# Kernel optimization log

Hardware: AMD Instinct MI355X
Metric: run time of the kernel (lower is better)

The kernel has to match this reference:

```python
import jax, jax.numpy as jnp
import numpy as np

K = 12          # number of agents (== max_other_agents, required by blowup)
MOA = 12        # max_other_agents
H, W, D = 24, 24, 8
C0, C1, C2, C3 = 32, 16, 16, 8
PHYS, MENT, ACT = 16, 16, 16
HSZ = C3 * H * W                      # 4608
INP = HSZ + PHYS + MENT + MOA * PHYS + MOA * MENT  # 5024
EPS = 1e-5
MIX = 0.9


def setup_inputs() -> dict:
    key = jax.random.key(0)
    ks = jax.random.split(key, 32)
    s = 0.02
    d = {
        "x": jax.random.normal(ks[0], (K, C0, D, H, W), jnp.float32),
        "p": jax.random.normal(ks[1], (K, PHYS), jnp.float32),
        "m": jax.random.normal(ks[2], (K, MENT), jnp.float32),
        "vis": jax.random.uniform(ks[3], (K, MOA), jnp.float32),
        "conv1_w": jax.random.normal(ks[4], (C1, C0, D), jnp.float32) * s,
        "conv1_b": jnp.zeros((C1,), jnp.float32),
        "bn1_g": jnp.ones((C1,), jnp.float32),
        "bn1_b": jnp.zeros((C1,), jnp.float32),
        "conv2_w": jax.random.normal(ks[5], (C2, C1, 3, 3), jnp.float32) * s,
        "conv2_b": jnp.zeros((C2,), jnp.float32),
        "bn2_g": jnp.ones((C2,), jnp.float32),
        "bn2_b": jnp.zeros((C2,), jnp.float32),
        "conv3_w": jax.random.normal(ks[6], (C3, C2, 5, 5), jnp.float32) * s,
        "conv3_b": jnp.zeros((C3,), jnp.float32),
        "bn3_g": jnp.ones((C3,), jnp.float32),
        "bn3_b": jnp.zeros((C3,), jnp.float32),
        "phys_w": jax.random.normal(ks[7], (PHYS, PHYS), jnp.float32) * s,
        "phys_b": jnp.zeros((PHYS,), jnp.float32),
        "ment_w": jax.random.normal(ks[8], (MENT, MENT), jnp.float32) * s,
        "ment_b": jnp.zeros((MENT,), jnp.float32),
        "w_ih": jax.random.normal(ks[9], (4 * HSZ, INP), jnp.float32) * s,
        "w_hh": jax.random.normal(ks[10], (4 * HSZ, HSZ), jnp.float32) * s,
        "b_ih": jnp.zeros((4 * HSZ,), jnp.float32),
        "b_hh": jnp.zeros((4 * HSZ,), jnp.float32),
        "ah_w": jax.random.normal(ks[11], (128, HSZ), jnp.float32) * s,
        "ah_b": jnp.zeros((128,), jnp.float32),
        "act_w": jax.random.normal(ks[12], (ACT, 128), jnp.float32) * s,
        "act_b": jnp.zeros((ACT,), jnp.float32),
        "inf_w": jax.random.normal(ks[13], (MOA * MENT, HSZ), jnp.float32) * s,
        "inf_b": jnp.zeros((MOA * MENT,), jnp.float32),
    }
    return d


def _bn2d(x, g, b):
    # batch-norm in training mode (batch statistics, biased var), x: [N,C,H,W]
    mu = jnp.mean(x, axis=(0, 2, 3), keepdims=True)
    var = jnp.mean((x - mu) ** 2, axis=(0, 2, 3), keepdims=True)
    return (x - mu) * jax.lax.rsqrt(var + EPS) * g[None, :, None, None] + b[None, :, None, None]


def _conv2d(x, w, b):
    y = jax.lax.conv_general_dilated(x, w, (1, 1), 'SAME',
                                     dimension_numbers=('NCHW', 'OIHW', 'NCHW'))
    return y + b[None, :, None, None]


def reference(x, p, m, vis,
              conv1_w, conv1_b, bn1_g, bn1_b,
              conv2_w, conv2_b, bn2_g, bn2_b,
              conv3_w, conv3_b, bn3_g, bn3_b,
              phys_w, phys_b, ment_w, ment_b,
              w_ih, w_hh, b_ih, b_hh,
              ah_w, ah_b, act_w, act_b, inf_w, inf_b):
    k = K
    # Conv3d with kernel (D,1,1) == contraction over channel and depth dims
    h1 = jnp.einsum('bcdhw,ocd->bohw', x, conv1_w) + conv1_b[None, :, None, None]
    h1 = jax.nn.relu(_bn2d(h1, bn1_g, bn1_b))          # [k,C1,H,W]
    h2 = jax.nn.relu(_bn2d(_conv2d(h1, conv2_w, conv2_b), bn2_g, bn2_b))
    h3 = jax.nn.relu(_bn2d(_conv2d(h2, conv3_w, conv3_b), bn3_g, bn3_b))  # [k,C3,H,W]

    ag = jnp.concatenate([jax.nn.relu(p @ phys_w.T + phys_b),
                          jax.nn.relu(m @ ment_w.T + ment_b)], axis=1)     # [k,PHYS+MENT]

    # blowup: broadcasted outer product (k == MOA so padding is a no-op)
    other_p = jax.nn.relu(p @ phys_w.T + phys_b)                           # [MOA,PHYS]
    phys_inp = vis[:, :, None] * other_p[None, :, :]                       # [k,MOA,PHYS]

    # mixed mental reps (old_ment is None on first step)
    other_m = MIX * jnp.broadcast_to(m[None, :, :], (k, MOA, MENT))
    ment_inp = jax.nn.relu(other_m.reshape(k * MOA, MENT) @ ment_w.T + ment_b)

    lstm_in = jnp.concatenate([h3.reshape(k, -1), ag,
                               phys_inp.reshape(k, -1),
                               ment_inp.reshape(k, -1)], axis=1)           # [k,INP]

    # single LSTM step with zero initial state (torch gate order i,f,g,o)
    gates = lstm_in @ w_ih.T + b_ih + b_hh                                 # h0 = 0
    i_g, f_g, g_g, o_g = jnp.split(gates, 4, axis=1)
    c = jax.nn.sigmoid(i_g) * jnp.tanh(g_g)                                # c0 = 0
    h = jax.nn.sigmoid(o_g) * jnp.tanh(c)                                  # [k,HSZ]

    hr = jax.nn.relu(h)
    old_ment = (hr @ inf_w.T + inf_b).reshape(k, MOA, MENT)
    act = jax.nn.relu(hr @ ah_w.T + ah_b) @ act_w.T + act_b               # [k,ACT]
    return act, old_ment
```

## Files before the change

kernel.cpp:

```cpp
#include <hip/hip_runtime.h>
#include <hip/hip_bf16.h>
#include <stdint.h>

typedef __hip_bfloat16 bf16;
typedef __attribute__((ext_vector_type(8))) short short8;
typedef __attribute__((ext_vector_type(4))) float floatx4;
typedef __attribute__((ext_vector_type(4))) float float4v;

#define DEV static __device__ __forceinline__

DEV float b2f(bf16 x) { return __bfloat162float(x); }
DEV float sb2f(short s) { return __uint_as_float(((unsigned int)(unsigned short)s) << 16); }
DEV short f2s(float f) { union { bf16 h; short s; } u; u.h = __float2bfloat16(f); return u.s; }
DEV float ld(const void* base, size_t idx, int f32) {
  return f32 ? ((const float*)base)[idx] : b2f(((const bf16*)base)[idx]);
}


static const size_t OFF_T1   = 0;
static const size_t OFF_T2   = 442368;
static const size_t OFF_T3   = 884736;
static const size_t OFF_BN1  = 1105920;
static const size_t OFF_BN2  = 1106048;
static const size_t OFF_BN3  = 1106176;
static const size_t OFF_PO   = 1106240;
static const size_t OFF_MA   = 1107008;
static const size_t OFF_MM   = 1107776;
static const size_t OFF_LSTM = 1108544;
static const size_t OFF_GATE = 1269312;
static const size_t OFF_HR   = 2154048;
static const size_t OFF_AH   = 2264640;
static const size_t OFF_FLAG = 2270784;

__global__ void k_detect(const unsigned int* __restrict__ g_raw, int* __restrict__ flag) {
  if (threadIdx.x == 0) *flag = (g_raw[0] == 0x3F800000u) ? 1 : 0;
}

__global__ __launch_bounds__(192) void k_conv1(const void* __restrict__ x,
                                               const void* __restrict__ w,
                                               const void* __restrict__ bias,
                                               float* __restrict__ t1,
                                               const int* __restrict__ flag) {
  int f32 = *flag;
  int b = blockIdx.x, og = blockIdx.y;
  __shared__ float wl[4][256];
  for (int i = threadIdx.x; i < 1024; i += 192) {
    int ol = i >> 8, cd = i & 255;
    wl[ol][cd] = ld(w, (size_t)(og * 4 + ol) * 256 + cd, f32);
  }
  __syncthreads();
  int tid = threadIdx.x;
  float acc[3][4];
#pragma unroll
  for (int p = 0; p < 3; ++p)
#pragma unroll
    for (int o = 0; o < 4; ++o) acc[p][o] = ld(bias, og * 4 + o, f32);
  size_t xb = (size_t)b * 256 * 576;
  for (int cd = 0; cd < 256; ++cd) {
    float x0 = ld(x, xb + cd * 576 + tid, f32);
    float x1 = ld(x, xb + cd * 576 + tid + 192, f32);
    float x2 = ld(x, xb + cd * 576 + tid + 384, f32);
#pragma unroll
    for (int o = 0; o < 4; ++o) {
      float wv = wl[o][cd];
      acc[0][o] += x0 * wv; acc[1][o] += x1 * wv; acc[2][o] += x2 * wv;
    }
  }
#pragma unroll
  for (int p = 0; p < 3; ++p)
#pragma unroll
    for (int o = 0; o < 4; ++o)
      t1[((size_t)b * 16 + og * 4 + o) * 576 + tid + p * 192] = acc[p][o];
}

__global__ __launch_bounds__(256) void k_bnstats(const float* __restrict__ src,
                                                 const void* __restrict__ g,
                                                 const void* __restrict__ bb,
                                                 float* __restrict__ prm, int C,
                                                 const int* __restrict__ flag) {
  int f32 = *flag;
  int c = blockIdx.x;
  float s = 0.f, s2 = 0.f;
  for (int i = threadIdx.x; i < 12 * 576; i += 256) {
    int b = i / 576, p = i % 576;
    float v = src[((size_t)b * C + c) * 576 + p];
    s += v; s2 += v * v;
  }
#pragma unroll
  for (int o = 1; o < 64; o <<= 1) { s += __shfl_xor(s, o, 64); s2 += __shfl_xor(s2, o, 64); }
  __shared__ float ls[4], ls2[4];
  int wv = threadIdx.x >> 6;
  if ((threadIdx.x & 63) == 0) { ls[wv] = s; ls2[wv] = s2; }
  __syncthreads();
  if (threadIdx.x == 0) {
    float S = ls[0] + ls[1] + ls[2] + ls[3];
    float S2 = ls2[0] + ls2[1] + ls2[2] + ls2[3];
    float mean = S * (1.f / 6912.f);
    float var = S2 * (1.f / 6912.f) - mean * mean;
    float sc = ld(g, c, f32) * rsqrtf(var + 1e-5f);
    prm[c * 2] = sc;
    prm[c * 2 + 1] = ld(bb, c, f32) - mean * sc;
  }
}

__global__ __launch_bounds__(256) void k_conv2(const float* __restrict__ t1,
                                               const float* __restrict__ bn1,
                                               const void* __restrict__ w,
                                               const void* __restrict__ bias,
                                               float* __restrict__ t2,
                                               const int* __restrict__ flag) {
  int f32 = *flag;
  int b = blockIdx.x, og = blockIdx.y;
  __shared__ float hin[16 * 676];
  __shared__ float wl[4 * 144];
  for (int i = threadIdx.x; i < 16 * 676; i += 256) hin[i] = 0.f;
  for (int i = threadIdx.x; i < 576; i += 256) wl[i] = ld(w, (size_t)og * 576 + i, f32);
  __syncthreads();
  for (int i = threadIdx.x; i < 16 * 576; i += 256) {
    int c = i / 576, p = i % 576, h = p / 24, wq = p % 24;
    float v = t1[((size_t)b * 16 + c) * 576 + p];
    v = v * bn1[c * 2] + bn1[c * 2 + 1];
    hin[c * 676 + (h + 1) * 26 + (wq + 1)] = fmaxf(v, 0.f);
  }
  __syncthreads();
  for (int it = threadIdx.x; it < 4 * 576; it += 256) {
    int ol = it / 576, p = it % 576, h = p / 24, wq = p % 24;
    float acc = ld(bias, og * 4 + ol, f32);
#pragma unroll
    for (int c = 0; c < 16; ++c) {
      const float* hp = &hin[c * 676 + h * 26 + wq];
      const float* wp = &wl[ol * 144 + c * 9];
#pragma unroll
      for (int ky = 0; ky < 3; ++ky)
#pragma unroll
        for (int kx = 0; kx < 3; ++kx)
          acc += hp[ky * 26 + kx] * wp[ky * 3 + kx];
    }
    t2[((size_t)b * 16 + og * 4 + ol) * 576 + p] = acc;
  }
}

__global__ __launch_bounds__(256) void k_conv3(const float* __restrict__ t2,
                                               const float* __restrict__ bn2,
                                               const void* __restrict__ w,
                                               const void* __restrict__ bias,
                                               float* __restrict__ t3,
                                               const int* __restrict__ flag) {
  int f32 = *flag;
  int b = blockIdx.x, og = blockIdx.y;
  __shared__ float hin[16 * 784];
  __shared__ float wl[2 * 400];
  for (int i = threadIdx.x; i < 16 * 784; i += 256) hin[i] = 0.f;
  for (int i = threadIdx.x; i < 800; i += 256) wl[i] = ld(w, (size_t)og * 800 + i, f32);
  __syncthreads();
  for (int i = threadIdx.x; i < 16 * 576; i += 256) {
    int c = i / 576, p = i % 576, h = p / 24, wq = p % 24;
    float v = t2[((size_t)b * 16 + c) * 576 + p];
    v = v * bn2[c * 2] + bn2[c * 2 + 1];
    hin[c * 784 + (h + 2) * 28 + (wq + 2)] = fmaxf(v, 0.f);
  }
  __syncthreads();
  for (int it = threadIdx.x; it < 2 * 576; it += 256) {
    int ol = it / 576, p = it % 576, h = p / 24, wq = p % 24;
    float acc = ld(bias, og * 2 + ol, f32);
#pragma unroll
    for (int c = 0; c < 16; ++c) {
      const float* hp = &hin[c * 784 + h * 28 + wq];
      const float* wp = &wl[ol * 400 + c * 25];
#pragma unroll
      for (int ky = 0; ky < 5; ++ky)
#pragma unroll
        for (int kx = 0; kx < 5; ++kx)
          acc += hp[ky * 28 + kx] * wp[ky * 5 + kx];
    }
    t3[((size_t)b * 8 + og * 2 + ol) * 576 + p] = acc;
  }
}

__global__ __launch_bounds__(192) void k_small(const void* __restrict__ p,
                                               const void* __restrict__ m,
                                               const void* __restrict__ pw,
                                               const void* __restrict__ pb,
                                               const void* __restrict__ mw,
                                               const void* __restrict__ mb,
                                               float* __restrict__ phys_out,
                                               float* __restrict__ ment_ag,
                                               float* __restrict__ mmv,
                                               const int* __restrict__ flag) {
  int f32 = *flag;
  int t = threadIdx.x;
  int j = t >> 4, o = t & 15;
  float a1 = ld(pb, o, f32), a2 = ld(mb, o, f32), a3 = ld(mb, o, f32);
#pragma unroll
  for (int i = 0; i < 16; ++i) {
    a1 += ld(p, j * 16 + i, f32) * ld(pw, o * 16 + i, f32);
    float mvv = ld(m, j * 16 + i, f32);
    float wvv = ld(mw, o * 16 + i, f32);
    a2 += mvv * wvv;
    a3 += 0.9f * mvv * wvv;
  }
  phys_out[t] = fmaxf(a1, 0.f);
  ment_ag[t] = fmaxf(a2, 0.f);
  mmv[t] = fmaxf(a3, 0.f);
}

__global__ __launch_bounds__(256) void k_assemble(const float* __restrict__ t3,
                                                  const float* __restrict__ bn3,
                                                  const float* __restrict__ phys_out,
                                                  const float* __restrict__ ment_ag,
                                                  const float* __restrict__ mmv,
                                                  const void* __restrict__ vis,
                                                  bf16* __restrict__ lstm_pad,
                                                  const int* __restrict__ flag) {
  int f32 = *flag;
  int idx = blockIdx.x * 256 + threadIdx.x;
  int mrow = idx / 5024, k = idx % 5024;
  float v = 0.f;
  if (mrow < 12) {
    if (k < 4608) {
      int c = k / 576, pos = k % 576;
      float t = t3[((size_t)mrow * 8 + c) * 576 + pos];
      v = fmaxf(t * bn3[c * 2] + bn3[c * 2 + 1], 0.f);
    } else if (k < 4624) {
      v = phys_out[mrow * 16 + (k - 4608)];
    } else if (k < 4640) {
      v = ment_ag[mrow * 16 + (k - 4624)];
    } else if (k < 4832) {
      int r = k - 4640;
      v = ld(vis, mrow * 12 + (r >> 4), f32) * phys_out[r];
    } else {
      v = mmv[k - 4832];
    }
  }
  lstm_pad[idx] = __float2bfloat16(v);
}

__global__ __launch_bounds__(128) void k_gemm(const bf16* __restrict__ lstm_pad,
                                              const void* __restrict__ w_ih,
                                              const void* __restrict__ b_ih,
                                              const void* __restrict__ b_hh,
                                              float* __restrict__ gates,
                                              const int* __restrict__ flag) {
  int f32 = *flag;
  __shared__ short8 A[2560];
  int tid = threadIdx.x;
  int wv = tid >> 6, lane = tid & 63;
  int jb0 = blockIdx.x * 32;
  int jr0 = (jb0 < 4608) ? jb0 : jb0 + 4608;
  int jl = jr0 + wv * 16 + (lane & 15);
  int quad = lane >> 4;
  floatx4 acc = {0.f, 0.f, 0.f, 0.f};
  const short* lp = (const short*)lstm_pad;
  const short* wp_base = (const short*)w_ih + (size_t)jl * 5024 + quad * 8;
  const float* wf_base = (const float*)w_ih + (size_t)jl * 5024 + quad * 8;
#pragma unroll 1
  for (int ph = 0; ph < 4; ++ph) {
    int kbase = ph * 1280;
    int KB = (ph < 3) ? 40 : 37;
    int nch = KB * 64;
    for (int c = tid; c < nch; c += 128) {
      int kb = c >> 6, r = c & 63, mr = r & 15, qc = (r >> 4) & 3;
      int k = kbase + kb * 32 + qc * 8;
      A[c] = *(const short8*)(lp + (size_t)mr * 5024 + k);
    }
    __syncthreads();
    if (!f32) {
      const short* wp = wp_base + kbase;
      for (int kb = 0; kb < KB; ++kb) {
        short8 av = A[kb * 64 + lane];
        short8 bv = *(const short8*)(wp + kb * 32);
        acc = __builtin_amdgcn_mfma_f32_16x16x32_bf16(av, bv, acc, 0, 0, 0);
      }
    } else {
      const float* wpf = wf_base + kbase;
      for (int kb = 0; kb < KB; ++kb) {
        short8 av = A[kb * 64 + lane];
        float4v w0 = *(const float4v*)(wpf + kb * 32);
        float4v w1 = *(const float4v*)(wpf + kb * 32 + 4);
        short8 bv;
        bv[0] = f2s(w0[0]); bv[1] = f2s(w0[1]); bv[2] = f2s(w0[2]); bv[3] = f2s(w0[3]);
        bv[4] = f2s(w1[0]); bv[5] = f2s(w1[1]); bv[6] = f2s(w1[2]); bv[7] = f2s(w1[3]);
        acc = __builtin_amdgcn_mfma_f32_16x16x32_bf16(av, bv, acc, 0, 0, 0);
      }
    }
    __syncthreads();
  }
  float bsum = ld(b_ih, jl, f32) + ld(b_hh, jl, f32);
#pragma unroll
  for (int q = 0; q < 4; ++q) {
    int mrow = quad * 4 + q;
    if (mrow < 12) gates[(size_t)mrow * 18432 + jl] = acc[q] + bsum;
  }
}

__global__ __launch_bounds__(256) void k_lstm(const float* __restrict__ gates,
                                              bf16* __restrict__ hr) {
  int idx = blockIdx.x * 256 + threadIdx.x;
  int mrow = idx / 4608, h = idx % 4608;
  const float* gm = gates + (size_t)mrow * 18432;
  float ig = gm[h], gg = gm[9216 + h], og = gm[13824 + h];
  float c = (1.f / (1.f + __expf(-ig))) * tanhf(gg);
  float hv = (1.f / (1.f + __expf(-og))) * tanhf(c);
  hr[idx] = __float2bfloat16(fmaxf(hv, 0.f));
}

__global__ __launch_bounds__(256) void k_heads(const bf16* __restrict__ hr,
                                               const void* __restrict__ inf_w,
                                               const void* __restrict__ inf_b,
                                               const void* __restrict__ ah_w,
                                               const void* __restrict__ ah_b,
                                               void* __restrict__ out,
                                               float* __restrict__ ah_ws,
                                               const int* __restrict__ flag) {
  int f32 = *flag;
  int gw = blockIdx.x * 4 + (threadIdx.x >> 6);
  int lane = threadIdx.x & 63;
  size_t wrow = (gw < 192) ? ((size_t)gw * 4608) : ((size_t)(gw - 192) * 4608);
  const void* wbase = (gw < 192) ? inf_w : ah_w;
  float acc[12];
#pragma unroll
  for (int q = 0; q < 12; ++q) acc[q] = 0.f;
  const short* hp = (const short*)hr;
  for (int it = 0; it < 9; ++it) {
    int k = it * 512 + lane * 8;
    float wf[8];
    if (f32) {
      const float* wrf = (const float*)wbase + wrow + k;
      float4v a0 = *(const float4v*)(wrf);
      float4v a1 = *(const float4v*)(wrf + 4);
      wf[0] = a0[0]; wf[1] = a0[1]; wf[2] = a0[2]; wf[3] = a0[3];
      wf[4] = a1[0]; wf[5] = a1[1]; wf[6] = a1[2]; wf[7] = a1[3];
    } else {
      short8 wv8 = *(const short8*)((const short*)wbase + wrow + k);
#pragma unroll
      for (int e = 0; e < 8; ++e) wf[e] = sb2f(wv8[e]);
    }
#pragma unroll
    for (int q = 0; q < 12; ++q) {
      short8 hv8 = *(const short8*)(hp + q * 4608 + k);
#pragma unroll
      for (int e = 0; e < 8; ++e)
        acc[q] += sb2f(hv8[e]) * wf[e];
    }
  }
#pragma unroll
  for (int s = 1; s < 64; s <<= 1)
#pragma unroll
    for (int q = 0; q < 12; ++q) acc[q] += __shfl_xor(acc[q], s, 64);
  float v = acc[0];
#pragma unroll
  for (int q = 1; q < 12; ++q)
    if (lane == q) v = acc[q];
  if (lane < 12) {
    if (gw < 192) {
      float v2 = v + ld(inf_b, gw, f32);
      size_t oi = 192 + (size_t)lane * 192 + gw;
      if (f32) ((float*)out)[oi] = v2;
      else ((bf16*)out)[oi] = __float2bfloat16(v2);
    } else {
      int a = gw - 192;
      ah_ws[lane * 128 + a] = fmaxf(v + ld(ah_b, a, f32), 0.f);
    }
  }
}

__global__ __launch_bounds__(256) void k_act(const float* __restrict__ ah_ws,
                                             const void* __restrict__ act_w,
                                             const void* __restrict__ act_b,
                                             void* __restrict__ out,
                                             const int* __restrict__ flag) {
  int f32 = *flag;
  int t = threadIdx.x;
  if (t < 192) {
    int mrow = t >> 4, a = t & 15;
    float acc = ld(act_b, a, f32);
    for (int c = 0; c < 128; ++c)
      acc += ah_ws[mrow * 128 + c] * ld(act_w, a * 128 + c, f32);
    if (f32) ((float*)out)[t] = acc;
    else ((bf16*)out)[t] = __float2bfloat16(acc);
  }
}

extern "C" void kernel_launch(void* const* d_in, const int* in_sizes, int n_in,
                              void* d_out, int out_size, void* d_ws, size_t ws_size,
                              hipStream_t stream) {
  const void* x       = d_in[0];
  const void* p       = d_in[1];
  const void* m       = d_in[2];
  const void* vis     = d_in[3];
  const void* conv1_w = d_in[4];
  const void* conv1_b = d_in[5];
  const void* bn1_g   = d_in[6];
  const void* bn1_b   = d_in[7];
  const void* conv2_w = d_in[8];
  const void* conv2_b = d_in[9];
  const void* bn2_g   = d_in[10];
  const void* bn2_b   = d_in[11];
  const void* conv3_w = d_in[12];
  const void* conv3_b = d_in[13];
  const void* bn3_g   = d_in[14];
  const void* bn3_b   = d_in[15];
  const void* phys_w  = d_in[16];
  const void* phys_b  = d_in[17];
  const void* ment_w  = d_in[18];
  const void* ment_b  = d_in[19];
  const void* w_ih    = d_in[20];
  const void* b_ih    = d_in[22];
  const void* b_hh    = d_in[23];
  const void* ah_w    = d_in[24];
  const void* ah_b    = d_in[25];
  const void* act_w   = d_in[26];
  const void* act_b   = d_in[27];
  const void* inf_w   = d_in[28];
  const void* inf_b   = d_in[29];

  char* ws = (char*)d_ws;
  float* t1       = (float*)(ws + OFF_T1);
  float* t2       = (float*)(ws + OFF_T2);
  float* t3       = (float*)(ws + OFF_T3);
  float* bn1p     = (float*)(ws + OFF_BN1);
  float* bn2p     = (float*)(ws + OFF_BN2);
  float* bn3p     = (float*)(ws + OFF_BN3);
  float* phys_out = (float*)(ws + OFF_PO);
  float* ment_ag  = (float*)(ws + OFF_MA);
  float* mmv      = (float*)(ws + OFF_MM);
  bf16* lstm_pad  = (bf16*)(ws + OFF_LSTM);
  float* gates    = (float*)(ws + OFF_GATE);
  bf16* hr        = (bf16*)(ws + OFF_HR);
  float* ah_ws    = (float*)(ws + OFF_AH);
  int*  dflag     = (int*)(ws + OFF_FLAG);

  k_detect<<<1, 64, 0, stream>>>((const unsigned int*)bn1_g, dflag);
  k_conv1<<<dim3(12, 4), 192, 0, stream>>>(x, conv1_w, conv1_b, t1, dflag);
  k_bnstats<<<16, 256, 0, stream>>>(t1, bn1_g, bn1_b, bn1p, 16, dflag);
  k_conv2<<<dim3(12, 4), 256, 0, stream>>>(t1, bn1p, conv2_w, conv2_b, t2, dflag);
  k_bnstats<<<16, 256, 0, stream>>>(t2, bn2_g, bn2_b, bn2p, 16, dflag);
  k_conv3<<<dim3(12, 4), 256, 0, stream>>>(t2, bn2p, conv3_w, conv3_b, t3, dflag);
  k_bnstats<<<8, 256, 0, stream>>>(t3, bn3_g, bn3_b, bn3p, 8, dflag);
  k_small<<<1, 192, 0, stream>>>(p, m, phys_w, phys_b, ment_w, ment_b,
                                 phys_out, ment_ag, mmv, dflag);
  k_assemble<<<314, 256, 0, stream>>>(t3, bn3p, phys_out, ment_ag, mmv, vis,
                                      lstm_pad, dflag);
  k_gemm<<<432, 128, 0, stream>>>(lstm_pad, w_ih, b_ih, b_hh, gates, dflag);
  k_lstm<<<216, 256, 0, stream>>>(gates, hr);
  k_heads<<<80, 256, 0, stream>>>(hr, inf_w, inf_b, ah_w, ah_b, d_out, ah_ws, dflag);
  k_act<<<1, 256, 0, stream>>>(ah_ws, act_w, act_b, d_out, dflag);
}
```

Before: 891.0 us.

## Fuse all stages into one persistent kernel with software grid barriers

Replaces the chain of thirteen kernel launches with a single persistent kernel of 216 blocks. Stages are separated by an atomic-counter grid barrier, and the dtype flag is detected inline instead of by a separate kernel. The aim is to remove per-launch overhead and inter-kernel gaps. The GEMM now runs on 216 blocks of 256 threads instead of 432 blocks of 128, and most blocks sit idle during the conv stages. The barrier assumes all blocks are co-resident and carries a spin timeout.

```diff
diff --git a/kernel.cpp b/kernel.cpp
--- a/kernel.cpp
+++ b/kernel.cpp
@@ -30,69 +30,51 @@
 static const size_t OFF_GATE = 1269312;
 static const size_t OFF_HR   = 2154048;
 static const size_t OFF_AH   = 2264640;
-static const size_t OFF_FLAG = 2270784;
-
-__global__ void k_detect(const unsigned int* __restrict__ g_raw, int* __restrict__ flag) {
-  if (threadIdx.x == 0) *flag = (g_raw[0] == 0x3F800000u) ? 1 : 0;
-}
-
-__global__ __launch_bounds__(192) void k_conv1(const void* __restrict__ x,
-                                               const void* __restrict__ w,
-                                               const void* __restrict__ bias,
-                                               float* __restrict__ t1,
-                                               const int* __restrict__ flag) {
-  int f32 = *flag;
-  int b = blockIdx.x, og = blockIdx.y;
-  __shared__ float wl[4][256];
-  for (int i = threadIdx.x; i < 1024; i += 192) {
-    int ol = i >> 8, cd = i & 255;
-    wl[ol][cd] = ld(w, (size_t)(og * 4 + ol) * 256 + cd, f32);
-  }
+static const size_t OFF_BAR  = 2270784;
+
+#define GRID 216
+
+union SmemU {
+  struct { float wl[4][256]; } c1;
+  struct { float hin[16 * 676]; float wl[4 * 144]; } c2;
+  struct { float hin[16 * 784]; float wl[2 * 400]; } c3;
+  short8 A[2560];
+};
+
+#define GSYNC()                                                                   \
+  do {                                                                            \
+    __syncthreads();                                                              \
+    ++bar_round;                                                                  \
+    if (tid == 0) {                                                               \
+      __threadfence();                                                            \
+      atomicAdd(bar, 1);                                                          \
+      int tgt = bar_round * GRID;                                                 \
+      int sp = 0;                                                                 \
+      while (__hip_atomic_load(bar, __ATOMIC_RELAXED,                             \
+                               __HIP_MEMORY_SCOPE_AGENT) < tgt) {                 \
+        __builtin_amdgcn_s_sleep(1);                                              \
+        if (++sp > 100000000) break;        \
+      }                                                                           \
+      __threadfence();                                                            \
+    }                                                                             \
+    __syncthreads();                                                              \
+  } while (0)
+
+DEV void bn_block(const float* __restrict__ src, const void* __restrict__ g,
+                  const void* __restrict__ bb, float* __restrict__ prm,
+                  int C, int c, int f32, float* ls, float* ls2, int tid) {
+  float s = 0.f, s2 = 0.f;
+  for (int i = tid; i < 12 * 576; i += 256) {
+    int b = i / 576, pq = i % 576;
+    float v = src[((size_t)b * C + c) * 576 + pq];
+    s += v; s2 += v * v;
+  }
+#pragma unroll
+  for (int o = 1; o < 64; o <<= 1) { s += __shfl_xor(s, o, 64); s2 += __shfl_xor(s2, o, 64); }
+  int wv = tid >> 6;
+  if ((tid & 63) == 0) { ls[wv] = s; ls2[wv] = s2; }
   __syncthreads();
-  int tid = threadIdx.x;
-  float acc[3][4];
-#pragma unroll
-  for (int p = 0; p < 3; ++p)
-#pragma unroll
-    for (int o = 0; o < 4; ++o) acc[p][o] = ld(bias, og * 4 + o, f32);
-  size_t xb = (size_t)b * 256 * 576;
-  for (int cd = 0; cd < 256; ++cd) {
-    float x0 = ld(x, xb + cd * 576 + tid, f32);
-    float x1 = ld(x, xb + cd * 576 + tid + 192, f32);
-    float x2 = ld(x, xb + cd * 576 + tid + 384, f32);
-#pragma unroll
-    for (int o = 0; o < 4; ++o) {
-      float wv = wl[o][cd];
-      acc[0][o] += x0 * wv; acc[1][o] += x1 * wv; acc[2][o] += x2 * wv;
-    }
-  }
-#pragma unroll
-  for (int p = 0; p < 3; ++p)
-#pragma unroll
-    for (int o = 0; o < 4; ++o)
-      t1[((size_t)b * 16 + og * 4 + o) * 576 + tid + p * 192] = acc[p][o];
-}
-
-__global__ __launch_bounds__(256) void k_bnstats(const float* __restrict__ src,
-                                                 const void* __restrict__ g,
-                                                 const void* __restrict__ bb,
-                                                 float* __restrict__ prm, int C,
-                                                 const int* __restrict__ flag) {
-  int f32 = *flag;
-  int c = blockIdx.x;
-  float s = 0.f, s2 = 0.f;
-  for (int i = threadIdx.x; i < 12 * 576; i += 256) {
-    int b = i / 576, p = i % 576;
-    float v = src[((size_t)b * C + c) * 576 + p];
-    s += v; s2 += v * v;
-  }
-#pragma unroll
-  for (int o = 1; o < 64; o <<= 1) { s += __shfl_xor(s, o, 64); s2 += __shfl_xor(s2, o, 64); }
-  __shared__ float ls[4], ls2[4];
-  int wv = threadIdx.x >> 6;
-  if ((threadIdx.x & 63) == 0) { ls[wv] = s; ls2[wv] = s2; }
-  __syncthreads();
-  if (threadIdx.x == 0) {
+  if (tid == 0) {
     float S = ls[0] + ls[1] + ls[2] + ls[3];
     float S2 = ls2[0] + ls2[1] + ls2[2] + ls2[3];
     float mean = S * (1.f / 6912.f);
@@ -103,281 +85,300 @@
   }
 }
 
-__global__ __launch_bounds__(256) void k_conv2(const float* __restrict__ t1,
-                                               const float* __restrict__ bn1,
-                                               const void* __restrict__ w,
-                                               const void* __restrict__ bias,
-                                               float* __restrict__ t2,
-                                               const int* __restrict__ flag) {
-  int f32 = *flag;
-  int b = blockIdx.x, og = blockIdx.y;
-  __shared__ float hin[16 * 676];
-  __shared__ float wl[4 * 144];
-  for (int i = threadIdx.x; i < 16 * 676; i += 256) hin[i] = 0.f;
-  for (int i = threadIdx.x; i < 576; i += 256) wl[i] = ld(w, (size_t)og * 576 + i, f32);
-  __syncthreads();
-  for (int i = threadIdx.x; i < 16 * 576; i += 256) {
-    int c = i / 576, p = i % 576, h = p / 24, wq = p % 24;
-    float v = t1[((size_t)b * 16 + c) * 576 + p];
-    v = v * bn1[c * 2] + bn1[c * 2 + 1];
-    hin[c * 676 + (h + 1) * 26 + (wq + 1)] = fmaxf(v, 0.f);
-  }
-  __syncthreads();
-  for (int it = threadIdx.x; it < 4 * 576; it += 256) {
-    int ol = it / 576, p = it % 576, h = p / 24, wq = p % 24;
-    float acc = ld(bias, og * 4 + ol, f32);
-#pragma unroll
-    for (int c = 0; c < 16; ++c) {
-      const float* hp = &hin[c * 676 + h * 26 + wq];
-      const float* wp = &wl[ol * 144 + c * 9];
-#pragma unroll
-      for (int ky = 0; ky < 3; ++ky)
-#pragma unroll
-        for (int kx = 0; kx < 3; ++kx)
-          acc += hp[ky * 26 + kx] * wp[ky * 3 + kx];
-    }
-    t2[((size_t)b * 16 + og * 4 + ol) * 576 + p] = acc;
-  }
-}
-
-__global__ __launch_bounds__(256) void k_conv3(const float* __restrict__ t2,
-                                               const float* __restrict__ bn2,
-                                               const void* __restrict__ w,
-                                               const void* __restrict__ bias,
-                                               float* __restrict__ t3,
-                                               const int* __restrict__ flag) {
-  int f32 = *flag;
-  int b = blockIdx.x, og = blockIdx.y;
-  __shared__ float hin[16 * 784];
-  __shared__ float wl[2 * 400];
-  for (int i = threadIdx.x; i < 16 * 784; i += 256) hin[i] = 0.f;
-  for (int i = threadIdx.x; i < 800; i += 256) wl[i] = ld(w, (size_t)og * 800 + i, f32);
-  __syncthreads();
-  for (int i = threadIdx.x; i < 16 * 576; i += 256) {
-    int c = i / 576, p = i % 576, h = p / 24, wq = p % 24;
-    float v = t2[((size_t)b * 16 + c) * 576 + p];
-    v = v * bn2[c * 2] + bn2[c * 2 + 1];
-    hin[c * 784 + (h + 2) * 28 + (wq + 2)] = fmaxf(v, 0.f);
-  }
-  __syncthreads();
-  for (int it = threadIdx.x; it < 2 * 576; it += 256) {
-    int ol = it / 576, p = it % 576, h = p / 24, wq = p % 24;
-    float acc = ld(bias, og * 2 + ol, f32);
-#pragma unroll
-    for (int c = 0; c < 16; ++c) {
-      const float* hp = &hin[c * 784 + h * 28 + wq];
-      const float* wp = &wl[ol * 400 + c * 25];
-#pragma unroll
-      for (int ky = 0; ky < 5; ++ky)
-#pragma unroll
-        for (int kx = 0; kx < 5; ++kx)
-          acc += hp[ky * 28 + kx] * wp[ky * 5 + kx];
-    }
-    t3[((size_t)b * 8 + og * 2 + ol) * 576 + p] = acc;
-  }
-}
-
-__global__ __launch_bounds__(192) void k_small(const void* __restrict__ p,
-                                               const void* __restrict__ m,
-                                               const void* __restrict__ pw,
-                                               const void* __restrict__ pb,
-                                               const void* __restrict__ mw,
-                                               const void* __restrict__ mb,
-                                               float* __restrict__ phys_out,
-                                               float* __restrict__ ment_ag,
-                                               float* __restrict__ mmv,
-                                               const int* __restrict__ flag) {
-  int f32 = *flag;
-  int t = threadIdx.x;
-  int j = t >> 4, o = t & 15;
-  float a1 = ld(pb, o, f32), a2 = ld(mb, o, f32), a3 = ld(mb, o, f32);
-#pragma unroll
-  for (int i = 0; i < 16; ++i) {
-    a1 += ld(p, j * 16 + i, f32) * ld(pw, o * 16 + i, f32);
-    float mvv = ld(m, j * 16 + i, f32);
-    float wvv = ld(mw, o * 16 + i, f32);
-    a2 += mvv * wvv;
-    a3 += 0.9f * mvv * wvv;
-  }
-  phys_out[t] = fmaxf(a1, 0.f);
-  ment_ag[t] = fmaxf(a2, 0.f);
-  mmv[t] = fmaxf(a3, 0.f);
-}
-
-__global__ __launch_bounds__(256) void k_assemble(const float* __restrict__ t3,
-                                                  const float* __restrict__ bn3,
-                                                  const float* __restrict__ phys_out,
-                                                  const float* __restrict__ ment_ag,
-                                                  const float* __restrict__ mmv,
-                                                  const void* __restrict__ vis,
-                                                  bf16* __restrict__ lstm_pad,
-                                                  const int* __restrict__ flag) {
-  int f32 = *flag;
-  int idx = blockIdx.x * 256 + threadIdx.x;
-  int mrow = idx / 5024, k = idx % 5024;
-  float v = 0.f;
-  if (mrow < 12) {
-    if (k < 4608) {
-      int c = k / 576, pos = k % 576;
-      float t = t3[((size_t)mrow * 8 + c) * 576 + pos];
-      v = fmaxf(t * bn3[c * 2] + bn3[c * 2 + 1], 0.f);
-    } else if (k < 4624) {
-      v = phys_out[mrow * 16 + (k - 4608)];
-    } else if (k < 4640) {
-      v = ment_ag[mrow * 16 + (k - 4624)];
-    } else if (k < 4832) {
-      int r = k - 4640;
-      v = ld(vis, mrow * 12 + (r >> 4), f32) * phys_out[r];
-    } else {
-      v = mmv[k - 4832];
-    }
-  }
-  lstm_pad[idx] = __float2bfloat16(v);
-}
-
-__global__ __launch_bounds__(128) void k_gemm(const bf16* __restrict__ lstm_pad,
-                                              const void* __restrict__ w_ih,
-                                              const void* __restrict__ b_ih,
-                                              const void* __restrict__ b_hh,
-                                              float* __restrict__ gates,
-                                              const int* __restrict__ flag) {
-  int f32 = *flag;
-  __shared__ short8 A[2560];
-  int tid = threadIdx.x;
-  int wv = tid >> 6, lane = tid & 63;
-  int jb0 = blockIdx.x * 32;
-  int jr0 = (jb0 < 4608) ? jb0 : jb0 + 4608;
-  int jl = jr0 + wv * 16 + (lane & 15);
-  int quad = lane >> 4;
-  floatx4 acc = {0.f, 0.f, 0.f, 0.f};
-  const short* lp = (const short*)lstm_pad;
-  const short* wp_base = (const short*)w_ih + (size_t)jl * 5024 + quad * 8;
-  const float* wf_base = (const float*)w_ih + (size_t)jl * 5024 + quad * 8;
+__global__ __launch_bounds__(256, 2) void k_all(
+    const void* __restrict__ x, const void* __restrict__ p,
+    const void* __restrict__ m, const void* __restrict__ vis,
+    const void* __restrict__ c1w, const void* __restrict__ c1b,
+    const void* __restrict__ g1, const void* __restrict__ b1,
+    const void* __restrict__ c2w, const void* __restrict__ c2b,
+    const void* __restrict__ g2, const void* __restrict__ b2,
+    const void* __restrict__ c3w, const void* __restrict__ c3b,
+    const void* __restrict__ g3, const void* __restrict__ b3,
+    const void* __restrict__ pw, const void* __restrict__ pb,
+    const void* __restrict__ mw, const void* __restrict__ mb,
+    const void* __restrict__ w_ih, const void* __restrict__ b_ih,
+    const void* __restrict__ b_hh,
+    const void* __restrict__ ah_w, const void* __restrict__ ah_b,
+    const void* __restrict__ act_w, const void* __restrict__ act_b,
+    const void* __restrict__ inf_w, const void* __restrict__ inf_b,
+    float* __restrict__ t1, float* __restrict__ t2, float* __restrict__ t3,
+    float* __restrict__ bn1p, float* __restrict__ bn2p, float* __restrict__ bn3p,
+    float* __restrict__ phys_out, float* __restrict__ ment_ag, float* __restrict__ mmv,
+    bf16* __restrict__ lstm_pad, float* __restrict__ gates, bf16* __restrict__ hr,
+    float* __restrict__ ah_ws, void* __restrict__ out, int* bar) {
+  __shared__ SmemU smem;
+  __shared__ float bnls[4], bnls2[4];
+  const int bid = blockIdx.x, tid = threadIdx.x;
+  const int f32 = (((const unsigned int*)g1)[0] == 0x3F800000u) ? 1 : 0;
+  int bar_round = 0;
+
+  if (bid < 48) {
+    int b = bid >> 2, og = bid & 3;
+    for (int i = tid; i < 1024; i += 256) {
+      int ol = i >> 8, cd = i & 255;
+      smem.c1.wl[ol][cd] = ld(c1w, (size_t)(og * 4 + ol) * 256 + cd, f32);
+    }
+    __syncthreads();
+    if (tid < 192) {
+      float acc[3][4];
+#pragma unroll
+      for (int pp = 0; pp < 3; ++pp)
+#pragma unroll
+        for (int o = 0; o < 4; ++o) acc[pp][o] = ld(c1b, og * 4 + o, f32);
+      size_t xb = (size_t)b * 256 * 576;
+      for (int cd = 0; cd < 256; ++cd) {
+        float x0 = ld(x, xb + cd * 576 + tid, f32);
+        float x1 = ld(x, xb + cd * 576 + tid + 192, f32);
+        float x2 = ld(x, xb + cd * 576 + tid + 384, f32);
+#pragma unroll
+        for (int o = 0; o < 4; ++o) {
+          float wv = smem.c1.wl[o][cd];
+          acc[0][o] += x0 * wv; acc[1][o] += x1 * wv; acc[2][o] += x2 * wv;
+        }
+      }
+#pragma unroll
+      for (int pp = 0; pp < 3; ++pp)
+#pragma unroll
+        for (int o = 0; o < 4; ++o)
+          t1[((size_t)b * 16 + og * 4 + o) * 576 + tid + pp * 192] = acc[pp][o];
+    }
+  }
+  GSYNC();
+
+  if (bid < 16) bn_block(t1, g1, b1, bn1p, 16, bid, f32, bnls, bnls2, tid);
+  GSYNC();
+
+  if (bid < 48) {
+    int b = bid >> 2, og = bid & 3;
+    float* hin = smem.c2.hin;
+    float* wl2 = smem.c2.wl;
+    for (int i = tid; i < 16 * 676; i += 256) hin[i] = 0.f;
+    for (int i = tid; i < 576; i += 256) wl2[i] = ld(c2w, (size_t)og * 576 + i, f32);
+    __syncthreads();
+    for (int i = tid; i < 16 * 576; i += 256) {
+      int c = i / 576, pq = i % 576, h = pq / 24, wq = pq % 24;
+      float v = t1[((size_t)b * 16 + c) * 576 + pq];
+      v = v * bn1p[c * 2] + bn1p[c * 2 + 1];
+      hin[c * 676 + (h + 1) * 26 + (wq + 1)] = fmaxf(v, 0.f);
+    }
+    __syncthreads();
+    for (int it = tid; it < 4 * 576; it += 256) {
+      int ol = it / 576, pq = it % 576, h = pq / 24, wq = pq % 24;
+      float acc = ld(c2b, og * 4 + ol, f32);
+#pragma unroll
+      for (int c = 0; c < 16; ++c) {
+        const float* hp = &hin[c * 676 + h * 26 + wq];
+        const float* wp2 = &wl2[ol * 144 + c * 9];
+#pragma unroll
+        for (int ky = 0; ky < 3; ++ky)
+#pragma unroll
+          for (int kx = 0; kx < 3; ++kx)
+            acc += hp[ky * 26 + kx] * wp2[ky * 3 + kx];
+      }
+      t2[((size_t)b * 16 + og * 4 + ol) * 576 + pq] = acc;
+    }
+  }
+  GSYNC();
+
+  if (bid < 16) bn_block(t2, g2, b2, bn2p, 16, bid, f32, bnls, bnls2, tid);
+  GSYNC();
+
+  if (bid < 48) {
+    int b = bid >> 2, og = bid & 3;
+    float* hin = smem.c3.hin;
+    float* wl3 = smem.c3.wl;
+    for (int i = tid; i < 16 * 784; i += 256) hin[i] = 0.f;
+    for (int i = tid; i < 800; i += 256) wl3[i] = ld(c3w, (size_t)og * 800 + i, f32);
+    __syncthreads();
+    for (int i = tid; i < 16 * 576; i += 256) {
+      int c = i / 576, pq = i % 576, h = pq / 24, wq = pq % 24;
+      float v = t2[((size_t)b * 16 + c) * 576 + pq];
+      v = v * bn2p[c * 2] + bn2p[c * 2 + 1];
+      hin[c * 784 + (h + 2) * 28 + (wq + 2)] = fmaxf(v, 0.f);
+    }
+    __syncthreads();
+    for (int it = tid; it < 2 * 576; it += 256) {
+      int ol = it / 576, pq = it % 576, h = pq / 24, wq = pq % 24;
+      float acc = ld(c3b, og * 2 + ol, f32);
+#pragma unroll
+      for (int c = 0; c < 16; ++c) {
+        const float* hp = &hin[c * 784 + h * 28 + wq];
+        const float* wp3 = &wl3[ol * 400 + c * 25];
+#pragma unroll
+        for (int ky = 0; ky < 5; ++ky)
+#pragma unroll
+          for (int kx = 0; kx < 5; ++kx)
+            acc += hp[ky * 28 + kx] * wp3[ky * 5 + kx];
+      }
+      t3[((size_t)b * 8 + og * 2 + ol) * 576 + pq] = acc;
+    }
+  }
+  GSYNC();
+
+  if (bid < 8) {
+    bn_block(t3, g3, b3, bn3p, 8, bid, f32, bnls, bnls2, tid);
+  } else if (bid == 8 && tid < 192) {
+    int j = tid >> 4, o = tid & 15;
+    float a1 = ld(pb, o, f32), a2 = ld(mb, o, f32), a3 = ld(mb, o, f32);
+#pragma unroll
+    for (int i = 0; i < 16; ++i) {
+      a1 += ld(p, j * 16 + i, f32) * ld(pw, o * 16 + i, f32);
+      float mvv = ld(m, j * 16 + i, f32);
+      float wvv = ld(mw, o * 16 + i, f32);
+      a2 += mvv * wvv;
+      a3 += 0.9f * mvv * wvv;
+    }
+    phys_out[tid] = fmaxf(a1, 0.f);
+    ment_ag[tid] = fmaxf(a2, 0.f);
+    mmv[tid] = fmaxf(a3, 0.f);
+  }
+  GSYNC();
+
+  for (int idx = bid * 256 + tid; idx < 80384; idx += GRID * 256) {
+    int mrow = idx / 5024, k = idx % 5024;
+    float v = 0.f;
+    if (mrow < 12) {
+      if (k < 4608) {
+        int c = k / 576, pos = k % 576;
+        float t = t3[((size_t)mrow * 8 + c) * 576 + pos];
+        v = fmaxf(t * bn3p[c * 2] + bn3p[c * 2 + 1], 0.f);
+      } else if (k < 4624) {
+        v = phys_out[mrow * 16 + (k - 4608)];
+      } else if (k < 4640) {
+        v = ment_ag[mrow * 16 + (k - 4624)];
+      } else if (k < 4832) {
+        int r = k - 4640;
+        v = ld(vis, mrow * 12 + (r >> 4), f32) * phys_out[r];
+      } else {
+        v = mmv[k - 4832];
+      }
+    }
+    lstm_pad[idx] = __float2bfloat16(v);
+  }
+  GSYNC();
+
+  {
+    int wv = tid >> 6, lane = tid & 63;
+    int jb0 = bid * 64;
+    int jr0 = (jb0 < 4608) ? jb0 : jb0 + 4608;
+    int jl = jr0 + wv * 16 + (lane & 15);
+    int quad = lane >> 4;
+    floatx4 acc = {0.f, 0.f, 0.f, 0.f};
+    const short* lp = (const short*)lstm_pad;
+    const short* wp_base = (const short*)w_ih + (size_t)jl * 5024 + quad * 8;
+    const float* wf_base = (const float*)w_ih + (size_t)jl * 5024 + quad * 8;
 #pragma unroll 1
-  for (int ph = 0; ph < 4; ++ph) {
-    int kbase = ph * 1280;
-    int KB = (ph < 3) ? 40 : 37;
-    int nch = KB * 64;
-    for (int c = tid; c < nch; c += 128) {
-      int kb = c >> 6, r = c & 63, mr = r & 15, qc = (r >> 4) & 3;
-      int k = kbase + kb * 32 + qc * 8;
-      A[c] = *(const short8*)(lp + (size_t)mr * 5024 + k);
-    }
-    __syncthreads();
-    if (!f32) {
-      const short* wp = wp_base + kbase;
-      for (int kb = 0; kb < KB; ++kb) {
-        short8 av = A[kb * 64 + lane];
-        short8 bv = *(const short8*)(wp + kb * 32);
-        acc = __builtin_amdgcn_mfma_f32_16x16x32_bf16(av, bv, acc, 0, 0, 0);
-      }
-    } else {
-      const float* wpf = wf_base + kbase;
-      for (int kb = 0; kb < KB; ++kb) {
-        short8 av = A[kb * 64 + lane];
-        float4v w0 = *(const float4v*)(wpf + kb * 32);
-        float4v w1 = *(const float4v*)(wpf + kb * 32 + 4);
-        short8 bv;
-        bv[0] = f2s(w0[0]); bv[1] = f2s(w0[1]); bv[2] = f2s(w0[2]); bv[3] = f2s(w0[3]);
-        bv[4] = f2s(w1[0]); bv[5] = f2s(w1[1]); bv[6] = f2s(w1[2]); bv[7] = f2s(w1[3]);
-        acc = __builtin_amdgcn_mfma_f32_16x16x32_bf16(av, bv, acc, 0, 0, 0);
-      }
-    }
-    __syncthreads();
-  }
-  float bsum = ld(b_ih, jl, f32) + ld(b_hh, jl, f32);
-#pragma unroll
-  for (int q = 0; q < 4; ++q) {
-    int mrow = quad * 4 + q;
-    if (mrow < 12) gates[(size_t)mrow * 18432 + jl] = acc[q] + bsum;
-  }
-}
-
-__global__ __launch_bounds__(256) void k_lstm(const float* __restrict__ gates,
-                                              bf16* __restrict__ hr) {
-  int idx = blockIdx.x * 256 + threadIdx.x;
-  int mrow = idx / 4608, h = idx % 4608;
-  const float* gm = gates + (size_t)mrow * 18432;
-  float ig = gm[h], gg = gm[9216 + h], og = gm[13824 + h];
-  float c = (1.f / (1.f + __expf(-ig))) * tanhf(gg);
-  float hv = (1.f / (1.f + __expf(-og))) * tanhf(c);
-  hr[idx] = __float2bfloat16(fmaxf(hv, 0.f));
-}
-
-__global__ __launch_bounds__(256) void k_heads(const bf16* __restrict__ hr,
-                                               const void* __restrict__ inf_w,
-                                               const void* __restrict__ inf_b,
-                                               const void* __restrict__ ah_w,
-                                               const void* __restrict__ ah_b,
-                                               void* __restrict__ out,
-                                               float* __restrict__ ah_ws,
-                                               const int* __restrict__ flag) {
-  int f32 = *flag;
-  int gw = blockIdx.x * 4 + (threadIdx.x >> 6);
-  int lane = threadIdx.x & 63;
-  size_t wrow = (gw < 192) ? ((size_t)gw * 4608) : ((size_t)(gw - 192) * 4608);
-  const void* wbase = (gw < 192) ? inf_w : ah_w;
-  float acc[12];
-#pragma unroll
-  for (int q = 0; q < 12; ++q) acc[q] = 0.f;
-  const short* hp = (const short*)hr;
-  for (int it = 0; it < 9; ++it) {
-    int k = it * 512 + lane * 8;
-    float wf[8];
-    if (f32) {
-      const float* wrf = (const float*)wbase + wrow + k;
-      float4v a0 = *(const float4v*)(wrf);
-      float4v a1 = *(const float4v*)(wrf + 4);
-      wf[0] = a0[0]; wf[1] = a0[1]; wf[2] = a0[2]; wf[3] = a0[3];
-      wf[4] = a1[0]; wf[5] = a1[1]; wf[6] = a1[2]; wf[7] = a1[3];
-    } else {
-      short8 wv8 = *(const short8*)((const short*)wbase + wrow + k);
-#pragma unroll
-      for (int e = 0; e < 8; ++e) wf[e] = sb2f(wv8[e]);
-    }
-#pragma unroll
-    for (int q = 0; q < 12; ++q) {
-      short8 hv8 = *(const short8*)(hp + q * 4608 + k);
-#pragma unroll
-      for (int e = 0; e < 8; ++e)
-        acc[q] += sb2f(hv8[e]) * wf[e];
-    }
-  }
-#pragma unroll
-  for (int s = 1; s < 64; s <<= 1)
-#pragma unroll
-    for (int q = 0; q < 12; ++q) acc[q] += __shfl_xor(acc[q], s, 64);
-  float v = acc[0];
-#pragma unroll
-  for (int q = 1; q < 12; ++q)
-    if (lane == q) v = acc[q];
-  if (lane < 12) {
-    if (gw < 192) {
-      float v2 = v + ld(inf_b, gw, f32);
-      size_t oi = 192 + (size_t)lane * 192 + gw;
-      if (f32) ((float*)out)[oi] = v2;
-      else ((bf16*)out)[oi] = __float2bfloat16(v2);
-    } else {
-      int a = gw - 192;
-      ah_ws[lane * 128 + a] = fmaxf(v + ld(ah_b, a, f32), 0.f);
-    }
-  }
-}
-
-__global__ __launch_bounds__(256) void k_act(const float* __restrict__ ah_ws,
-                                             const void* __restrict__ act_w,
-                                             const void* __restrict__ act_b,
-                                             void* __restrict__ out,
-                                             const int* __restrict__ flag) {
-  int f32 = *flag;
-  int t = threadIdx.x;
-  if (t < 192) {
-    int mrow = t >> 4, a = t & 15;
+    for (int ph = 0; ph < 4; ++ph) {
+      int kbase = ph * 1280;
+      int KB = (ph < 3) ? 40 : 37;
+      int nch = KB * 64;
+      for (int c = tid; c < nch; c += 256) {
+        int kb = c >> 6, r = c & 63, mr = r & 15, qc = (r >> 4) & 3;
+        int k = kbase + kb * 32 + qc * 8;
+        smem.A[c] = *(const short8*)(lp + (size_t)mr * 5024 + k);
+      }
+      __syncthreads();
+      if (!f32) {
+        const short* wp = wp_base + kbase;
+        for (int kb = 0; kb < KB; ++kb) {
+          short8 av = smem.A[kb * 64 + lane];
+          short8 bv = *(const short8*)(wp + kb * 32);
+          acc = __builtin_amdgcn_mfma_f32_16x16x32_bf16(av, bv, acc, 0, 0, 0);
+        }
+      } else {
+        const float* wpf = wf_base + kbase;
+        for (int kb = 0; kb < KB; ++kb) {
+          short8 av = smem.A[kb * 64 + lane];
+          float4v w0 = *(const float4v*)(wpf + kb * 32);
+          float4v w1 = *(const float4v*)(wpf + kb * 32 + 4);
+          short8 bv;
+          bv[0] = f2s(w0[0]); bv[1] = f2s(w0[1]); bv[2] = f2s(w0[2]); bv[3] = f2s(w0[3]);
+          bv[4] = f2s(w1[0]); bv[5] = f2s(w1[1]); bv[6] = f2s(w1[2]); bv[7] = f2s(w1[3]);
+          acc = __builtin_amdgcn_mfma_f32_16x16x32_bf16(av, bv, acc, 0, 0, 0);
+        }
+      }
+      __syncthreads();
+    }
+    float bsum = ld(b_ih, jl, f32) + ld(b_hh, jl, f32);
+#pragma unroll
+    for (int q = 0; q < 4; ++q) {
+      int mrow2 = quad * 4 + q;
+      if (mrow2 < 12) gates[(size_t)mrow2 * 18432 + jl] = acc[q] + bsum;
+    }
+  }
+  GSYNC();
+
+  {
+    int idx = bid * 256 + tid;
+    int mrow = idx / 4608, h = idx % 4608;
+    const float* gm = gates + (size_t)mrow * 18432;
+    float ig = gm[h], gg = gm[9216 + h], og2 = gm[13824 + h];
+    float c = (1.f / (1.f + __expf(-ig))) * tanhf(gg);
+    float hv = (1.f / (1.f + __expf(-og2))) * tanhf(c);
+    hr[idx] = __float2bfloat16(fmaxf(hv, 0.f));
+  }
+  GSYNC();
+
+  if (bid < 80) {
+    int gw = bid * 4 + (tid >> 6);
+    int lane = tid & 63;
+    size_t wrow = (gw < 192) ? ((size_t)gw * 4608) : ((size_t)(gw - 192) * 4608);
+    const void* wbase = (gw < 192) ? inf_w : ah_w;
+    float acc[12];
+#pragma unroll
+    for (int q = 0; q < 12; ++q) acc[q] = 0.f;
+    const short* hp = (const short*)hr;
+    for (int it = 0; it < 9; ++it) {
+      int k = it * 512 + lane * 8;
+      float wf[8];
+      if (f32) {
+        const float* wrf = (const float*)wbase + wrow + k;
+        float4v a0 = *(const float4v*)(wrf);
+        float4v a1 = *(const float4v*)(wrf + 4);
+        wf[0] = a0[0]; wf[1] = a0[1]; wf[2] = a0[2]; wf[3] = a0[3];
+        wf[4] = a1[0]; wf[5] = a1[1]; wf[6] = a1[2]; wf[7] = a1[3];
+      } else {
+        short8 wv8 = *(const short8*)((const short*)wbase + wrow + k);
+#pragma unroll
+        for (int e = 0; e < 8; ++e) wf[e] = sb2f(wv8[e]);
+      }
+#pragma unroll
+      for (int q = 0; q < 12; ++q) {
+        short8 hv8 = *(const short8*)(hp + q * 4608 + k);
+#pragma unroll
+        for (int e = 0; e < 8; ++e)
+          acc[q] += sb2f(hv8[e]) * wf[e];
+      }
+    }
+#pragma unroll
+    for (int s = 1; s < 64; s <<= 1)
+#pragma unroll
+      for (int q = 0; q < 12; ++q) acc[q] += __shfl_xor(acc[q], s, 64);
+    float v = acc[0];
+#pragma unroll
+    for (int q = 1; q < 12; ++q)
+      if (lane == q) v = acc[q];
+    if (lane < 12) {
+      if (gw < 192) {
+        float v2 = v + ld(inf_b, gw, f32);
+        size_t oi = 192 + (size_t)lane * 192 + gw;
+        if (f32) ((float*)out)[oi] = v2;
+        else ((bf16*)out)[oi] = __float2bfloat16(v2);
+      } else {
+        int a = gw - 192;
+        ah_ws[lane * 128 + a] = fmaxf(v + ld(ah_b, a, f32), 0.f);
+      }
+    }
+  }
+  GSYNC();
+
+  if (bid == 0 && tid < 192) {
+    int mrow = tid >> 4, a = tid & 15;
     float acc = ld(act_b, a, f32);
     for (int c = 0; c < 128; ++c)
       acc += ah_ws[mrow * 128 + c] * ld(act_w, a * 128 + c, f32);
-    if (f32) ((float*)out)[t] = acc;
-    else ((bf16*)out)[t] = __float2bfloat16(acc);
+    if (f32) ((float*)out)[tid] = acc;
+    else ((bf16*)out)[tid] = __float2bfloat16(acc);
   }
 }
 
@@ -428,21 +429,14 @@
   float* gates    = (float*)(ws + OFF_GATE);
   bf16* hr        = (bf16*)(ws + OFF_HR);
   float* ah_ws    = (float*)(ws + OFF_AH);
-  int*  dflag     = (int*)(ws + OFF_FLAG);
-
-  k_detect<<<1, 64, 0, stream>>>((const unsigned int*)bn1_g, dflag);
-  k_conv1<<<dim3(12, 4), 192, 0, stream>>>(x, conv1_w, conv1_b, t1, dflag);
-  k_bnstats<<<16, 256, 0, stream>>>(t1, bn1_g, bn1_b, bn1p, 16, dflag);
-  k_conv2<<<dim3(12, 4), 256, 0, stream>>>(t1, bn1p, conv2_w, conv2_b, t2, dflag);
-  k_bnstats<<<16, 256, 0, stream>>>(t2, bn2_g, bn2_b, bn2p, 16, dflag);
-  k_conv3<<<dim3(12, 4), 256, 0, stream>>>(t2, bn2p, conv3_w, conv3_b, t3, dflag);
-  k_bnstats<<<8, 256, 0, stream>>>(t3, bn3_g, bn3_b, bn3p, 8, dflag);
-  k_small<<<1, 192, 0, stream>>>(p, m, phys_w, phys_b, ment_w, ment_b,
-                                 phys_out, ment_ag, mmv, dflag);
-  k_assemble<<<314, 256, 0, stream>>>(t3, bn3p, phys_out, ment_ag, mmv, vis,
-                                      lstm_pad, dflag);
-  k_gemm<<<432, 128, 0, stream>>>(lstm_pad, w_ih, b_ih, b_hh, gates, dflag);
-  k_lstm<<<216, 256, 0, stream>>>(gates, hr);
-  k_heads<<<80, 256, 0, stream>>>(hr, inf_w, inf_b, ah_w, ah_b, d_out, ah_ws, dflag);
-  k_act<<<1, 256, 0, stream>>>(ah_ws, act_w, act_b, d_out, dflag);
+  int*  bar       = (int*)(ws + OFF_BAR);
+
+  hipMemsetAsync(bar, 0, 8, stream);
+  k_all<<<dim3(GRID), dim3(256), 0, stream>>>(
+      x, p, m, vis, conv1_w, conv1_b, bn1_g, bn1_b,
+      conv2_w, conv2_b, bn2_g, bn2_b, conv3_w, conv3_b, bn3_g, bn3_b,
+      phys_w, phys_b, ment_w, ment_b, w_ih, b_ih, b_hh,
+      ah_w, ah_b, act_w, act_b, inf_w, inf_b,
+      t1, t2, t3, bn1p, bn2p, bn3p, phys_out, ment_ag, mmv,
+      lstm_pad, gates, hr, ah_ws, d_out, bar);
 }
```

Result: slower. 980.8 us (+10.1%).
